# Performance work log

Hardware: AMD Instinct MI355X
Metric: run time of the kernel (lower is better)

The kernel has to match this reference:

```python
import jax, jax.numpy as jnp
import numpy as np

N = 10000      # nodes
E = 320000     # edges (avg degree 32)
IN = 512       # in_channels
OUT = 128      # out_channels
H = 4          # in_head
C1 = 2 * OUT   # per-head hidden channels of conv1 (256)
NEG_SLOPE = 0.2


def setup_inputs() -> dict:
    key = jax.random.key(0)
    ks = jax.random.split(key, 12)
    x = jax.random.normal(ks[0], (N, IN), dtype=jnp.float32)
    edge_index = jax.random.randint(ks[1], (2, E), 0, N, dtype=jnp.int64)
    def glorot(k, shape):
        lim = np.sqrt(6.0 / (shape[0] + shape[-1])).astype(np.float32)
        return jax.random.uniform(k, shape, jnp.float32, -lim, lim)
    # conv1: GATv2Conv(IN -> C1 per head, heads=H)
    Wl1 = glorot(ks[2], (IN, H * C1))
    Wr1 = glorot(ks[3], (IN, H * C1))
    att1 = glorot(ks[4], (H, C1))
    b1 = jnp.zeros((H * C1,), jnp.float32)
    # conv2: GATv2Conv(H*C1 -> OUT, heads=1)
    Wl2 = glorot(ks[5], (H * C1, OUT))
    Wr2 = glorot(ks[6], (H * C1, OUT))
    att2 = glorot(ks[7], (1, OUT))
    b2 = jnp.zeros((OUT,), jnp.float32)
    return {"x": x, "edge_index": edge_index, "Wl1": Wl1, "Wr1": Wr1,
            "att1": att1, "b1": b1, "Wl2": Wl2, "Wr2": Wr2,
            "att2": att2, "b2": b2}


def gatv2_conv(x, src, dst, Wl, Wr, att, b, heads, ch):
    # x: [N, F_in]; src/dst: [E] (message src -> dst, softmax over dst)
    n = x.shape[0]
    xl = (x @ Wl).reshape(n, heads, ch)   # source-side projection
    xr = (x @ Wr).reshape(n, heads, ch)   # target-side projection
    # per-edge GATv2 score: att . LeakyReLU(xl_j + xr_i)   [E, H]
    e = jax.nn.leaky_relu(xl[src] + xr[dst], NEG_SLOPE)    # [E, H, C]
    s = jnp.einsum('ehc,hc->eh', e, att)                   # [E, H]
    # segment softmax over incoming edges of each dst node
    smax = jax.lax.stop_gradient(jax.ops.segment_max(s, dst, num_segments=n))
    ex = jnp.exp(s - smax[dst])
    denom = jax.ops.segment_sum(ex, dst, num_segments=n)
    alpha = ex / denom[dst]                                # [E, H]
    # weighted scatter-add of source messages
    out = jax.ops.segment_sum(alpha[:, :, None] * xl[src], dst, num_segments=n)
    return out.reshape(n, heads * ch) + b                  # concat heads + bias


def reference(x, edge_index, Wl1, Wr1, att1, b1, Wl2, Wr2, att2, b2):
    src, dst = edge_index[0], edge_index[1]
    h = gatv2_conv(x, src, dst, Wl1, Wr1, att1, b1, H, C1)
    h = jax.nn.relu(h)                                     # [N, H*C1]
    out = gatv2_conv(h, src, dst, Wl2, Wr2, att2, b2, 1, OUT)
    return out                                             # [N, OUT]
```

## Files before the change

kernel.cpp:

```cpp
#include <hip/hip_runtime.h>
#include <cfloat>

#define N_NODES 10000
#define N_EDGES 320000
#define IN_F    512
#define F1      1024
#define OUT_F   128
#define NEG     0.2f
#define BUCKET  128

typedef __attribute__((ext_vector_type(8))) short bf16x8;
typedef __attribute__((ext_vector_type(4))) float f32x4;

__device__ __forceinline__ float lrelu(float v) { return fmaxf(v, NEG * v); }

__device__ __forceinline__ unsigned short f2bf(float f) {
    unsigned u = __float_as_uint(f);
    u += 0x7fff + ((u >> 16) & 1);
    return (unsigned short)(u >> 16);
}
__device__ __forceinline__ float bf2f(unsigned short h) {
    return __uint_as_float(((unsigned)h) << 16);
}
__device__ __forceinline__ void u2f2(unsigned u, float& e0, float& e1) {
    e0 = __uint_as_float(u << 16);
    e1 = __uint_as_float(u & 0xffff0000u);
}

__device__ __forceinline__ void gld_lds16(const void* g, void* l) {
    __builtin_amdgcn_global_load_lds(
        (const __attribute__((address_space(1))) unsigned int*)g,
        (__attribute__((address_space(3))) unsigned int*)l, 16, 0, 0);
}

#define PB_X  2500
#define PB_S  3750
#define PB_W1 4774
#define PB_END 5030

__device__ __forceinline__ void wt_body(const float* __restrict__ Wa,
                                        const float* __restrict__ Wb,
                                        unsigned short* __restrict__ tbf,
                                        int K, int NS, int n0, int k0, int t,
                                        float (*tile)[33]) {
    int j = t & 31;
    const float* W = (n0 < NS) ? Wa : Wb;
    int nb = (n0 < NS) ? n0 : n0 - NS;
#pragma unroll
    for (int r = 0; r < 4; ++r) {
        int kl = (t >> 5) + r * 8;
        tile[kl][j] = W[(size_t)(k0 + kl) * NS + nb + j];
    }
    __syncthreads();
#pragma unroll
    for (int r = 0; r < 4; ++r) {
        int nl = (t >> 5) + r * 8;
        tbf[(size_t)(n0 + nl) * K + k0 + j] = f2bf(tile[j][nl]);
    }
}

__global__ __launch_bounds__(256) void k_prep(const float* __restrict__ x,
                                              unsigned short* __restrict__ xbf,
                                              const int* __restrict__ ei,
                                              int* __restrict__ cnt,
                                              int* __restrict__ esrc,
                                              const float* __restrict__ Wl1,
                                              const float* __restrict__ Wr1,
                                              unsigned short* __restrict__ w1bf,
                                              const float* __restrict__ Wl2,
                                              const float* __restrict__ Wr2,
                                              unsigned short* __restrict__ w2bf) {
    __shared__ float tile[32][33];
    int bid = blockIdx.x, t = threadIdx.x;
    if (bid < PB_X) {
        int i = bid * 2048 + t * 8;
        float4 v0 = *(const float4*)(x + i);
        float4 v1 = *(const float4*)(x + i + 4);
        ushort4 h0, h1;
        h0.x = f2bf(v0.x); h0.y = f2bf(v0.y); h0.z = f2bf(v0.z); h0.w = f2bf(v0.w);
        h1.x = f2bf(v1.x); h1.y = f2bf(v1.y); h1.z = f2bf(v1.z); h1.w = f2bf(v1.w);
        *(ushort4*)(xbf + i) = h0;
        *(ushort4*)(xbf + i + 4) = h1;
    } else if (bid < PB_S) {
        int e = (bid - PB_X) * 256 + t;
        if (e < N_EDGES) {
            int d = ei[N_EDGES + e];
            int pos = atomicAdd(&cnt[d], 1);
            if (pos < BUCKET) esrc[(size_t)d * BUCKET + pos] = ei[e];
        }
    } else if (bid < PB_W1) {
        int local = bid - PB_S;
        wt_body(Wl1, Wr1, w1bf, IN_F, F1, (local & 63) * 32, (local >> 6) * 32, t, tile);
    } else {
        int local = bid - PB_W1;
        wt_body(Wl2, Wr2, w2bf, F1, OUT_F, (local & 7) * 32, (local >> 3) * 32, t, tile);
    }
}

template<int BM, int WR, int WC>
__global__ __launch_bounds__(256) void gemm_mfma(
        const unsigned short* __restrict__ A,
        const unsigned short* __restrict__ B,
        unsigned short* __restrict__ Cl, unsigned short* __restrict__ Cr,
        int M, int K, int NSPLIT) {
    constexpr int NI = BM / (16 * WR);
    constexpr int NJ = 128 / (16 * WC);
    __shared__ __align__(16) short As[BM * 32];
    __shared__ __align__(16) short Bs[128 * 32];
    int t = threadIdx.x;
    int lane = t & 63, w = t >> 6;
    int row0 = blockIdx.y * BM;
    int n0 = blockIdx.x * 128;
    int wr0 = (w / WC) * (NI * 16);
    int wc0 = (w % WC) * (NJ * 16);
    int q = lane >> 4, md = lane & 15;
    int srow = t >> 2;
    int skoff = (t & 3) * 8;

    f32x4 acc[NI][NJ];
#pragma unroll
    for (int i = 0; i < NI; ++i)
#pragma unroll
        for (int j = 0; j < NJ; ++j)
#pragma unroll
            for (int r = 0; r < 4; ++r) acc[i][j][r] = 0.f;

    for (int k0 = 0; k0 < K; k0 += 32) {
        __syncthreads();
#pragma unroll
        for (int is = 0; is < BM / 64; ++is) {
            int gr = row0 + is * 64 + srow;
            if (gr < M)
                gld_lds16(A + (size_t)gr * K + k0 + skoff,
                          &As[(is * 64 + (t >> 6) * 16) * 32]);
        }
#pragma unroll
        for (int is = 0; is < 2; ++is) {
            int gn = n0 + is * 64 + srow;
            gld_lds16(B + (size_t)gn * K + k0 + skoff,
                      &Bs[(is * 64 + (t >> 6) * 16) * 32]);
        }
        __syncthreads();

        bf16x8 av[NI], bv[NJ];
#pragma unroll
        for (int i = 0; i < NI; ++i)
            av[i] = *(const bf16x8*)&As[(wr0 + i * 16 + md) * 32 + q * 8];
#pragma unroll
        for (int j = 0; j < NJ; ++j)
            bv[j] = *(const bf16x8*)&Bs[(wc0 + j * 16 + md) * 32 + q * 8];
#pragma unroll
        for (int i = 0; i < NI; ++i)
#pragma unroll
            for (int j = 0; j < NJ; ++j)
                acc[i][j] = __builtin_amdgcn_mfma_f32_16x16x32_bf16(av[i], bv[j], acc[i][j], 0, 0, 0);
    }

#pragma unroll
    for (int i = 0; i < NI; ++i)
#pragma unroll
        for (int j = 0; j < NJ; ++j) {
            int col = n0 + wc0 + j * 16 + md;
            unsigned short* C = (col < NSPLIT) ? Cl : Cr;
            int cc = (col < NSPLIT) ? col : col - NSPLIT;
#pragma unroll
            for (int r = 0; r < 4; ++r) {
                int grow = row0 + wr0 + i * 16 + q * 4 + r;
                if (grow < M) C[(size_t)grow * NSPLIT + cc] = f2bf(acc[i][j][r]);
            }
        }
}

__global__ __launch_bounds__(256) void k_fused1(const unsigned short* __restrict__ xlbf,
                                                const unsigned short* __restrict__ xrbf,
                                                const int* __restrict__ cnt,
                                                const int* __restrict__ esrc,
                                                const float* __restrict__ att,
                                                const float* __restrict__ bias,
                                                unsigned short* __restrict__ hb) {
    int t = threadIdx.x;
    int w = t >> 6, lane = t & 63;
    int ni = w >> 1;
    int ww = w & 1;
    int nd = blockIdx.x * 2 + ni;
    int head = lane >> 4, sub = lane & 15;
    int ch = head * 256 + sub * 16;

    __shared__ float slx[4][4];
    __shared__ float4 sacc4[2][4][64];

    float4 r0, r1, r2, r3;
    {
        const uint4* prx = (const uint4*)(xrbf + (size_t)nd * F1 + ch);
        uint4 xa = prx[0], xb = prx[1];
        u2f2(xa.x, r0.x, r0.y); u2f2(xa.y, r0.z, r0.w);
        u2f2(xa.z, r1.x, r1.y); u2f2(xa.w, r1.z, r1.w);
        u2f2(xb.x, r2.x, r2.y); u2f2(xb.y, r2.z, r2.w);
        u2f2(xb.z, r3.x, r3.y); u2f2(xb.w, r3.z, r3.w);
    }
    const float4* pa = (const float4*)(att + ch);
    float4 a0 = pa[0], a1 = pa[1], a2 = pa[2], a3 = pa[3];

    int deg = min(cnt[nd], BUCKET);
    int p0 = nd * BUCKET;
    int half = (deg + 1) >> 1;
    int pa_ = p0 + (ww ? half : 0);
    int pb_ = p0 + (ww ? deg : half);

    float l = 0.f;
    float4 acc0 = make_float4(0.f, 0.f, 0.f, 0.f);
    float4 acc1 = acc0, acc2 = acc0, acc3 = acc0;

    uint4 ua, ub;
    if (pa_ < pb_) {
        const uint4* pv = (const uint4*)(xlbf + (size_t)esrc[pa_] * F1 + ch);
        ua = pv[0]; ub = pv[1];
    }
    for (int p = pa_; p < pb_; ++p) {
        uint4 ca = ua, cb = ub;
        if (p + 1 < pb_) {
            const uint4* pv = (const uint4*)(xlbf + (size_t)esrc[p + 1] * F1 + ch);
            ua = pv[0]; ub = pv[1];
        }
        float4 c0, c1, c2, c3;
        u2f2(ca.x, c0.x, c0.y); u2f2(ca.y, c0.z, c0.w);
        u2f2(ca.z, c1.x, c1.y); u2f2(ca.w, c1.z, c1.w);
        u2f2(cb.x, c2.x, c2.y); u2f2(cb.y, c2.z, c2.w);
        u2f2(cb.z, c3.x, c3.y); u2f2(cb.w, c3.z, c3.w);
        float s0, s1, s2, s3;
        s0 = a0.x * lrelu(c0.x + r0.x);
        s0 = fmaf(a0.y, lrelu(c0.y + r0.y), s0);
        s0 = fmaf(a0.z, lrelu(c0.z + r0.z), s0);
        s0 = fmaf(a0.w, lrelu(c0.w + r0.w), s0);
        s1 = a1.x * lrelu(c1.x + r1.x);
        s1 = fmaf(a1.y, lrelu(c1.y + r1.y), s1);
        s1 = fmaf(a1.z, lrelu(c1.z + r1.z), s1);
        s1 = fmaf(a1.w, lrelu(c1.w + r1.w), s1);
        s2 = a2.x * lrelu(c2.x + r2.x);
        s2 = fmaf(a2.y, lrelu(c2.y + r2.y), s2);
        s2 = fmaf(a2.z, lrelu(c2.z + r2.z), s2);
        s2 = fmaf(a2.w, lrelu(c2.w + r2.w), s2);
        s3 = a3.x * lrelu(c3.x + r3.x);
        s3 = fmaf(a3.y, lrelu(c3.y + r3.y), s3);
        s3 = fmaf(a3.z, lrelu(c3.z + r3.z), s3);
        s3 = fmaf(a3.w, lrelu(c3.w + r3.w), s3);
        float s = (s0 + s1) + (s2 + s3);
#pragma unroll
        for (int off = 1; off < 16; off <<= 1) s += __shfl_xor(s, off);
        s = fminf(fmaxf(s, -60.f), 60.f);
        float al = __expf(s);
        l += al;
        acc0.x = fmaf(al, c0.x, acc0.x);
        acc0.y = fmaf(al, c0.y, acc0.y);
        acc0.z = fmaf(al, c0.z, acc0.z);
        acc0.w = fmaf(al, c0.w, acc0.w);
        acc1.x = fmaf(al, c1.x, acc1.x);
        acc1.y = fmaf(al, c1.y, acc1.y);
        acc1.z = fmaf(al, c1.z, acc1.z);
        acc1.w = fmaf(al, c1.w, acc1.w);
        acc2.x = fmaf(al, c2.x, acc2.x);
        acc2.y = fmaf(al, c2.y, acc2.y);
        acc2.z = fmaf(al, c2.z, acc2.z);
        acc2.w = fmaf(al, c2.w, acc2.w);
        acc3.x = fmaf(al, c3.x, acc3.x);
        acc3.y = fmaf(al, c3.y, acc3.y);
        acc3.z = fmaf(al, c3.z, acc3.z);
        acc3.w = fmaf(al, c3.w, acc3.w);
    }

    if (sub == 0) slx[w][head] = l;
    if (ww == 1) {
        sacc4[ni][0][lane] = acc0;
        sacc4[ni][1][lane] = acc1;
        sacc4[ni][2][lane] = acc2;
        sacc4[ni][3][lane] = acc3;
    }
    __syncthreads();
    if (ww == 0) {
        float L = l + slx[w ^ 1][head];
        float invL = (L > 0.f) ? 1.f / L : 0.f;
        const float4* pb = (const float4*)(bias + ch);
        size_t base = (size_t)nd * F1 + ch;
        float4 aa[4] = {acc0, acc1, acc2, acc3};
#pragma unroll
        for (int j = 0; j < 4; ++j) {
            float4 pt = sacc4[ni][j][lane];
            float4 b4 = pb[j];
            ushort4 hv;
            hv.x = f2bf(fmaxf(fmaf(aa[j].x + pt.x, invL, b4.x), 0.f));
            hv.y = f2bf(fmaxf(fmaf(aa[j].y + pt.y, invL, b4.y), 0.f));
            hv.z = f2bf(fmaxf(fmaf(aa[j].z + pt.z, invL, b4.z), 0.f));
            hv.w = f2bf(fmaxf(fmaf(aa[j].w + pt.w, invL, b4.w), 0.f));
            *(ushort4*)(hb + base + j * 4) = hv;
        }
    }
}

__global__ __launch_bounds__(256) void k_fused2(const unsigned short* __restrict__ xlbf,
                                                const unsigned short* __restrict__ xrbf,
                                                const int* __restrict__ cnt,
                                                const int* __restrict__ esrc,
                                                const float* __restrict__ att,
                                                const float* __restrict__ bias,
                                                float* __restrict__ out) {
    int t = threadIdx.x;
    int w = t >> 6, lane = t & 63;
    int nd = blockIdx.x * 4 + w;
    int g = lane >> 4, sub = lane & 15;
    int ch = sub * 8;

    __shared__ float slx2[4][4];
    __shared__ float sacc2[4][4][132];

    float r[8], a[8];
    {
        uint4 u = *(const uint4*)(xrbf + (size_t)nd * OUT_F + ch);
        u2f2(u.x, r[0], r[1]); u2f2(u.y, r[2], r[3]);
        u2f2(u.z, r[4], r[5]); u2f2(u.w, r[6], r[7]);
        float4 q0 = *(const float4*)(att + ch);
        float4 q1 = *(const float4*)(att + ch + 4);
        a[0] = q0.x; a[1] = q0.y; a[2] = q0.z; a[3] = q0.w;
        a[4] = q1.x; a[5] = q1.y; a[6] = q1.z; a[7] = q1.w;
    }
    int deg = min(cnt[nd], BUCKET);
    int p0 = nd * BUCKET;
    int p1 = p0 + deg;

    float l = 0.f;
    float acc[8] = {};
    uint4 cur, nxt;
    {
        int p = p0 + g;
        if (p < p1)     cur = *(const uint4*)(xlbf + (size_t)esrc[p] * OUT_F + ch);
        if (p + 4 < p1) nxt = *(const uint4*)(xlbf + (size_t)esrc[p + 4] * OUT_F + ch);
    }
    for (int p = p0 + g; p < p1; p += 4) {
        uint4 c = cur;
        cur = nxt;
        if (p + 8 < p1) nxt = *(const uint4*)(xlbf + (size_t)esrc[p + 8] * OUT_F + ch);
        float v[8];
        u2f2(c.x, v[0], v[1]); u2f2(c.y, v[2], v[3]);
        u2f2(c.z, v[4], v[5]); u2f2(c.w, v[6], v[7]);
        float sx = a[0] * lrelu(v[0] + r[0]);
        sx = fmaf(a[1], lrelu(v[1] + r[1]), sx);
        sx = fmaf(a[2], lrelu(v[2] + r[2]), sx);
        sx = fmaf(a[3], lrelu(v[3] + r[3]), sx);
        float sy = a[4] * lrelu(v[4] + r[4]);
        sy = fmaf(a[5], lrelu(v[5] + r[5]), sy);
        sy = fmaf(a[6], lrelu(v[6] + r[6]), sy);
        sy = fmaf(a[7], lrelu(v[7] + r[7]), sy);
        float s = sx + sy;
#pragma unroll
        for (int off = 1; off < 16; off <<= 1) s += __shfl_xor(s, off);
        s = fminf(fmaxf(s, -60.f), 60.f);
        float al = __expf(s);
        l += al;
#pragma unroll
        for (int k = 0; k < 8; ++k) acc[k] = fmaf(al, v[k], acc[k]);
    }

    if (sub == 0) slx2[w][g] = l;
    float4 v0 = make_float4(acc[0], acc[1], acc[2], acc[3]);
    float4 v1 = make_float4(acc[4], acc[5], acc[6], acc[7]);
    *(float4*)&sacc2[w][g][ch] = v0;
    *(float4*)&sacc2[w][g][ch + 4] = v1;
    __syncthreads();
    float L = slx2[w][0] + slx2[w][1] + slx2[w][2] + slx2[w][3];
    float invL = (L > 0.f) ? 1.f / L : 0.f;
    int c2 = lane * 2;
    float o0 = sacc2[w][0][c2] + sacc2[w][1][c2] + sacc2[w][2][c2] + sacc2[w][3][c2];
    float o1 = sacc2[w][0][c2 + 1] + sacc2[w][1][c2 + 1] + sacc2[w][2][c2 + 1] + sacc2[w][3][c2 + 1];
    float2 bf = *(const float2*)(bias + c2);
    float2 o;
    o.x = fmaf(o0, invL, bf.x);
    o.y = fmaf(o1, invL, bf.y);
    *(float2*)(out + (size_t)nd * OUT_F + c2) = o;
}

extern "C" void kernel_launch(void* const* d_in, const int* in_sizes, int n_in,
                              void* d_out, int out_size, void* d_ws, size_t ws_size,
                              hipStream_t stream) {
    const float* x    = (const float*)d_in[0];
    const int*   ei   = (const int*)d_in[1];
    const float* Wl1  = (const float*)d_in[2];
    const float* Wr1  = (const float*)d_in[3];
    const float* att1 = (const float*)d_in[4];
    const float* b1   = (const float*)d_in[5];
    const float* Wl2  = (const float*)d_in[6];
    const float* Wr2  = (const float*)d_in[7];
    const float* att2 = (const float*)d_in[8];
    const float* b2   = (const float*)d_in[9];
    float* out = (float*)d_out;

    unsigned short* us = (unsigned short*)d_ws;
    unsigned short* xl1bf = us;
    unsigned short* xr1bf = xl1bf + (size_t)N_NODES * F1;
    unsigned short* xl2bf = xr1bf + (size_t)N_NODES * F1;
    unsigned short* xr2bf = xl2bf + (size_t)N_NODES * OUT_F;
    unsigned short* hb   = xr2bf + (size_t)N_NODES * OUT_F;
    unsigned short* xbf  = hb + (size_t)N_NODES * F1;
    unsigned short* w1bf = xbf + (size_t)N_NODES * IN_F;
    unsigned short* w2bf = w1bf + (size_t)2048 * IN_F;
    int* cnt   = (int*)(w2bf + (size_t)256 * F1);
    int* esrc  = cnt + (N_NODES + 16);

    hipMemsetAsync(cnt, 0, sizeof(int) * N_NODES, stream);
    k_prep<<<PB_END, 256, 0, stream>>>(x, xbf, ei, cnt, esrc,
                                       Wl1, Wr1, w1bf,
                                       Wl2, Wr2, w2bf);

    gemm_mfma<128, 2, 2><<<dim3(16, (N_NODES + 127) / 128), 256, 0, stream>>>(
        xbf, w1bf, xl1bf, xr1bf, N_NODES, IN_F, F1);

    k_fused1<<<N_NODES / 2, 256, 0, stream>>>(xl1bf, xr1bf, cnt, esrc, att1, b1, hb);

    gemm_mfma<64, 1, 4><<<dim3(2, (N_NODES + 63) / 64), 256, 0, stream>>>(
        hb, w2bf, xl2bf, xr2bf, N_NODES, F1, OUT_F);

    k_fused2<<<N_NODES / 4, 256, 0, stream>>>(xl2bf, xr2bf, cnt, esrc, att2, b2, out);
}
```

Measured before the change: 264.8 us.

## Decompose LeakyReLU score into per-node dot terms plus abs term in conv1

Rewrites the conv1 attention score using lrelu(v)=0.6v+0.4|v|. The linear part becomes a per-source dot product, computed once per node in a new k_pq1 kernel, plus a per-destination term computed once in the fused kernel, so the per-edge loop only needs an abs-weighted sum. It also replaces the shuffle reductions with DPP row reductions, goes from two waves per node to one wave per node (dropping the LDS combine and barrier), and deepens the gather prefetch to two edges. The cost is an extra small kernel launch and the loss of intra-node edge parallelism for high-degree nodes.

```diff
diff --git a/kernel.cpp b/kernel.cpp
--- a/kernel.cpp
+++ b/kernel.cpp
@@ -25,6 +25,14 @@
 __device__ __forceinline__ void u2f2(unsigned u, float& e0, float& e1) {
     e0 = __uint_as_float(u << 16);
     e1 = __uint_as_float(u & 0xffff0000u);
+}
+
+__device__ __forceinline__ float rsum16(float x) {
+    x += __int_as_float(__builtin_amdgcn_update_dpp(0, __float_as_int(x), 0x121, 0xF, 0xF, false));
+    x += __int_as_float(__builtin_amdgcn_update_dpp(0, __float_as_int(x), 0x122, 0xF, 0xF, false));
+    x += __int_as_float(__builtin_amdgcn_update_dpp(0, __float_as_int(x), 0x124, 0xF, 0xF, false));
+    x += __int_as_float(__builtin_amdgcn_update_dpp(0, __float_as_int(x), 0x128, 0xF, 0xF, false));
+    return x;
 }
 
 __device__ __forceinline__ void gld_lds16(const void* g, void* l) {
@@ -171,23 +179,48 @@
         }
 }
 
+__global__ __launch_bounds__(256) void k_pq1(const unsigned short* __restrict__ xlbf,
+                                             const float* __restrict__ att,
+                                             float* __restrict__ P) {
+    int t = threadIdx.x;
+    int w = t >> 6, lane = t & 63;
+    int nd = blockIdx.x * 4 + w;
+    int head = lane >> 4, sub = lane & 15;
+    int ch = head * 256 + sub * 16;
+    const uint4* px = (const uint4*)(xlbf + (size_t)nd * F1 + ch);
+    uint4 xa = px[0], xb = px[1];
+    const float4* pa = (const float4*)(att + ch);
+    float4 a0 = pa[0], a1 = pa[1], a2 = pa[2], a3 = pa[3];
+    float4 c0, c1, c2, c3;
+    u2f2(xa.x, c0.x, c0.y); u2f2(xa.y, c0.z, c0.w);
+    u2f2(xa.z, c1.x, c1.y); u2f2(xa.w, c1.z, c1.w);
+    u2f2(xb.x, c2.x, c2.y); u2f2(xb.y, c2.z, c2.w);
+    u2f2(xb.z, c3.x, c3.y); u2f2(xb.w, c3.z, c3.w);
+    float s0 = a0.x * c0.x;
+    s0 = fmaf(a0.y, c0.y, s0); s0 = fmaf(a0.z, c0.z, s0); s0 = fmaf(a0.w, c0.w, s0);
+    float s1 = a1.x * c1.x;
+    s1 = fmaf(a1.y, c1.y, s1); s1 = fmaf(a1.z, c1.z, s1); s1 = fmaf(a1.w, c1.w, s1);
+    float s2 = a2.x * c2.x;
+    s2 = fmaf(a2.y, c2.y, s2); s2 = fmaf(a2.z, c2.z, s2); s2 = fmaf(a2.w, c2.w, s2);
+    float s3 = a3.x * c3.x;
+    s3 = fmaf(a3.y, c3.y, s3); s3 = fmaf(a3.z, c3.z, s3); s3 = fmaf(a3.w, c3.w, s3);
+    float s = rsum16((s0 + s1) + (s2 + s3));
+    if (sub == 0) P[nd * 4 + head] = s;
+}
+
 __global__ __launch_bounds__(256) void k_fused1(const unsigned short* __restrict__ xlbf,
                                                 const unsigned short* __restrict__ xrbf,
                                                 const int* __restrict__ cnt,
                                                 const int* __restrict__ esrc,
                                                 const float* __restrict__ att,
+                                                const float* __restrict__ Pbuf,
                                                 const float* __restrict__ bias,
                                                 unsigned short* __restrict__ hb) {
     int t = threadIdx.x;
     int w = t >> 6, lane = t & 63;
-    int ni = w >> 1;
-    int ww = w & 1;
-    int nd = blockIdx.x * 2 + ni;
+    int nd = blockIdx.x * 4 + w;
     int head = lane >> 4, sub = lane & 15;
     int ch = head * 256 + sub * 16;
-
-    __shared__ float slx[4][4];
-    __shared__ float4 sacc4[2][4][64];
 
     float4 r0, r1, r2, r3;
     {
@@ -201,54 +234,71 @@
     const float4* pa = (const float4*)(att + ch);
     float4 a0 = pa[0], a1 = pa[1], a2 = pa[2], a3 = pa[3];
 
+    float qd = a0.x * r0.x;
+    qd = fmaf(a0.y, r0.y, qd); qd = fmaf(a0.z, r0.z, qd); qd = fmaf(a0.w, r0.w, qd);
+    qd = fmaf(a1.x, r1.x, qd); qd = fmaf(a1.y, r1.y, qd);
+    qd = fmaf(a1.z, r1.z, qd); qd = fmaf(a1.w, r1.w, qd);
+    qd = fmaf(a2.x, r2.x, qd); qd = fmaf(a2.y, r2.y, qd);
+    qd = fmaf(a2.z, r2.z, qd); qd = fmaf(a2.w, r2.w, qd);
+    qd = fmaf(a3.x, r3.x, qd); qd = fmaf(a3.y, r3.y, qd);
+    qd = fmaf(a3.z, r3.z, qd); qd = fmaf(a3.w, r3.w, qd);
+    float Qk = 0.6f * rsum16(qd);
+
     int deg = min(cnt[nd], BUCKET);
     int p0 = nd * BUCKET;
-    int half = (deg + 1) >> 1;
-    int pa_ = p0 + (ww ? half : 0);
-    int pb_ = p0 + (ww ? deg : half);
+    int p1 = p0 + deg;
 
     float l = 0.f;
     float4 acc0 = make_float4(0.f, 0.f, 0.f, 0.f);
     float4 acc1 = acc0, acc2 = acc0, acc3 = acc0;
 
-    uint4 ua, ub;
-    if (pa_ < pb_) {
-        const uint4* pv = (const uint4*)(xlbf + (size_t)esrc[pa_] * F1 + ch);
-        ua = pv[0]; ub = pv[1];
-    }
-    for (int p = pa_; p < pb_; ++p) {
-        uint4 ca = ua, cb = ub;
-        if (p + 1 < pb_) {
-            const uint4* pv = (const uint4*)(xlbf + (size_t)esrc[p + 1] * F1 + ch);
-            ua = pv[0]; ub = pv[1];
+    uint4 A0 = {}, B0 = {}, A1 = {}, B1 = {};
+    float Pv0 = 0.f, Pv1 = 0.f;
+    if (p0 < p1) {
+        int sn = esrc[p0];
+        const uint4* pv = (const uint4*)(xlbf + (size_t)sn * F1 + ch);
+        A0 = pv[0]; B0 = pv[1]; Pv0 = Pbuf[sn * 4 + head];
+    }
+    if (p0 + 1 < p1) {
+        int sn = esrc[p0 + 1];
+        const uint4* pv = (const uint4*)(xlbf + (size_t)sn * F1 + ch);
+        A1 = pv[0]; B1 = pv[1]; Pv1 = Pbuf[sn * 4 + head];
+    }
+    for (int p = p0; p < p1; ++p) {
+        uint4 ca = A0, cb = B0;
+        float Pv = Pv0;
+        A0 = A1; B0 = B1; Pv0 = Pv1;
+        if (p + 2 < p1) {
+            int sn = esrc[p + 2];
+            const uint4* pv = (const uint4*)(xlbf + (size_t)sn * F1 + ch);
+            A1 = pv[0]; B1 = pv[1]; Pv1 = Pbuf[sn * 4 + head];
         }
         float4 c0, c1, c2, c3;
         u2f2(ca.x, c0.x, c0.y); u2f2(ca.y, c0.z, c0.w);
         u2f2(ca.z, c1.x, c1.y); u2f2(ca.w, c1.z, c1.w);
         u2f2(cb.x, c2.x, c2.y); u2f2(cb.y, c2.z, c2.w);
         u2f2(cb.z, c3.x, c3.y); u2f2(cb.w, c3.z, c3.w);
-        float s0, s1, s2, s3;
-        s0 = a0.x * lrelu(c0.x + r0.x);
-        s0 = fmaf(a0.y, lrelu(c0.y + r0.y), s0);
-        s0 = fmaf(a0.z, lrelu(c0.z + r0.z), s0);
-        s0 = fmaf(a0.w, lrelu(c0.w + r0.w), s0);
-        s1 = a1.x * lrelu(c1.x + r1.x);
-        s1 = fmaf(a1.y, lrelu(c1.y + r1.y), s1);
-        s1 = fmaf(a1.z, lrelu(c1.z + r1.z), s1);
-        s1 = fmaf(a1.w, lrelu(c1.w + r1.w), s1);
-        s2 = a2.x * lrelu(c2.x + r2.x);
-        s2 = fmaf(a2.y, lrelu(c2.y + r2.y), s2);
-        s2 = fmaf(a2.z, lrelu(c2.z + r2.z), s2);
-        s2 = fmaf(a2.w, lrelu(c2.w + r2.w), s2);
-        s3 = a3.x * lrelu(c3.x + r3.x);
-        s3 = fmaf(a3.y, lrelu(c3.y + r3.y), s3);
-        s3 = fmaf(a3.z, lrelu(c3.z + r3.z), s3);
-        s3 = fmaf(a3.w, lrelu(c3.w + r3.w), s3);
-        float s = (s0 + s1) + (s2 + s3);
-#pragma unroll
-        for (int off = 1; off < 16; off <<= 1) s += __shfl_xor(s, off);
-        s = fminf(fmaxf(s, -60.f), 60.f);
-        float al = __expf(s);
+        float s0 = a0.x * fabsf(c0.x + r0.x);
+        s0 = fmaf(a0.y, fabsf(c0.y + r0.y), s0);
+        s0 = fmaf(a0.z, fabsf(c0.z + r0.z), s0);
+        s0 = fmaf(a0.w, fabsf(c0.w + r0.w), s0);
+        float s1 = a1.x * fabsf(c1.x + r1.x);
+        s1 = fmaf(a1.y, fabsf(c1.y + r1.y), s1);
+        s1 = fmaf(a1.z, fabsf(c1.z + r1.z), s1);
+        s1 = fmaf(a1.w, fabsf(c1.w + r1.w), s1);
+        float s2 = a2.x * fabsf(c2.x + r2.x);
+        s2 = fmaf(a2.y, fabsf(c2.y + r2.y), s2);
+        s2 = fmaf(a2.z, fabsf(c2.z + r2.z), s2);
+        s2 = fmaf(a2.w, fabsf(c2.w + r2.w), s2);
+        float s3 = a3.x * fabsf(c3.x + r3.x);
+        s3 = fmaf(a3.y, fabsf(c3.y + r3.y), s3);
+        s3 = fmaf(a3.z, fabsf(c3.z + r3.z), s3);
+        s3 = fmaf(a3.w, fabsf(c3.w + r3.w), s3);
+        float sab = rsum16((s0 + s1) + (s2 + s3));
+        float sarg = fmaf(0.6f, Pv, Qk);
+        sarg = fmaf(0.4f, sab, sarg);
+        sarg = fminf(fmaxf(sarg, -60.f), 60.f);
+        float al = __expf(sarg);
         l += al;
         acc0.x = fmaf(al, c0.x, acc0.x);
         acc0.y = fmaf(al, c0.y, acc0.y);
@@ -268,31 +318,19 @@
         acc3.w = fmaf(al, c3.w, acc3.w);
     }
 
-    if (sub == 0) slx[w][head] = l;
-    if (ww == 1) {
-        sacc4[ni][0][lane] = acc0;
-        sacc4[ni][1][lane] = acc1;
-        sacc4[ni][2][lane] = acc2;
-        sacc4[ni][3][lane] = acc3;
-    }
-    __syncthreads();
-    if (ww == 0) {
-        float L = l + slx[w ^ 1][head];
-        float invL = (L > 0.f) ? 1.f / L : 0.f;
-        const float4* pb = (const float4*)(bias + ch);
-        size_t base = (size_t)nd * F1 + ch;
-        float4 aa[4] = {acc0, acc1, acc2, acc3};
-#pragma unroll
-        for (int j = 0; j < 4; ++j) {
-            float4 pt = sacc4[ni][j][lane];
-            float4 b4 = pb[j];
-            ushort4 hv;
-            hv.x = f2bf(fmaxf(fmaf(aa[j].x + pt.x, invL, b4.x), 0.f));
-            hv.y = f2bf(fmaxf(fmaf(aa[j].y + pt.y, invL, b4.y), 0.f));
-            hv.z = f2bf(fmaxf(fmaf(aa[j].z + pt.z, invL, b4.z), 0.f));
-            hv.w = f2bf(fmaxf(fmaf(aa[j].w + pt.w, invL, b4.w), 0.f));
-            *(ushort4*)(hb + base + j * 4) = hv;
-        }
+    float invL = (l > 0.f) ? 1.f / l : 0.f;
+    const float4* pb = (const float4*)(bias + ch);
+    size_t base = (size_t)nd * F1 + ch;
+    float4 aa[4] = {acc0, acc1, acc2, acc3};
+#pragma unroll
+    for (int j = 0; j < 4; ++j) {
+        float4 b4 = pb[j];
+        ushort4 hv;
+        hv.x = f2bf(fmaxf(fmaf(aa[j].x, invL, b4.x), 0.f));
+        hv.y = f2bf(fmaxf(fmaf(aa[j].y, invL, b4.y), 0.f));
+        hv.z = f2bf(fmaxf(fmaf(aa[j].z, invL, b4.z), 0.f));
+        hv.w = f2bf(fmaxf(fmaf(aa[j].w, invL, b4.w), 0.f));
+        *(ushort4*)(hb + base + j * 4) = hv;
     }
 }
 
@@ -349,9 +387,7 @@
         sy = fmaf(a[5], lrelu(v[5] + r[5]), sy);
         sy = fmaf(a[6], lrelu(v[6] + r[6]), sy);
         sy = fmaf(a[7], lrelu(v[7] + r[7]), sy);
-        float s = sx + sy;
-#pragma unroll
-        for (int off = 1; off < 16; off <<= 1) s += __shfl_xor(s, off);
+        float s = rsum16(sx + sy);
         s = fminf(fmaxf(s, -60.f), 60.f);
         float al = __expf(s);
         l += al;
@@ -403,6 +439,7 @@
     unsigned short* w2bf = w1bf + (size_t)2048 * IN_F;
     int* cnt   = (int*)(w2bf + (size_t)256 * F1);
     int* esrc  = cnt + (N_NODES + 16);
+    float* Pbuf = (float*)(esrc + (size_t)N_NODES * BUCKET);
 
     hipMemsetAsync(cnt, 0, sizeof(int) * N_NODES, stream);
     k_prep<<<PB_END, 256, 0, stream>>>(x, xbf, ei, cnt, esrc,
@@ -412,7 +449,9 @@
     gemm_mfma<128, 2, 2><<<dim3(16, (N_NODES + 127) / 128), 256, 0, stream>>>(
         xbf, w1bf, xl1bf, xr1bf, N_NODES, IN_F, F1);
 
-    k_fused1<<<N_NODES / 2, 256, 0, stream>>>(xl1bf, xr1bf, cnt, esrc, att1, b1, hb);
+    k_pq1<<<N_NODES / 4, 256, 0, stream>>>(xl1bf, att1, Pbuf);
+
+    k_fused1<<<N_NODES / 4, 256, 0, stream>>>(xl1bf, xr1bf, cnt, esrc, att1, Pbuf, b1, hb);
 
     gemm_mfma<64, 1, 4><<<dim3(2, (N_NODES + 63) / 64), 256, 0, stream>>>(
         hb, w2bf, xl2bf, xr2bf, N_NODES, F1, OUT_F);
```

Measured after the change: 278.3 us. +5.1%, slower.
